# Optimization experiments

Hardware: AMD Instinct MI355X
Metric: run time of the kernel (lower is better)

Reference implementation:

```python
import jax, jax.numpy as jnp
import numpy as np

B, S, D, H, FF = 2, 2048, 1024, 16, 4096
HD = D // H
SCALE = 1.0 / np.sqrt(HD).astype(np.float32)
EPS = 1e-5


def _ln(x, g, b):
    m = jnp.mean(x, axis=-1, keepdims=True)
    v = jnp.mean((x - m) ** 2, axis=-1, keepdims=True)
    return (x - m) * jax.lax.rsqrt(v + EPS) * g + b


def setup_inputs() -> dict:
    key = jax.random.key(0)
    ks = jax.random.split(key, 8)
    def lin(k, fan_in, shape):
        return (jax.random.normal(k, shape, jnp.float32) / np.sqrt(fan_in)).astype(jnp.float32)
    return {
        "x": jax.random.normal(ks[0], (B, S, D), jnp.float32),
        "w_qkv": lin(ks[1], D, (D, 3 * D)),          # qkv_proj (no bias)
        "w_o": lin(ks[2], D, (D, D)),                 # out_proj
        "b_o": jnp.zeros((D,), jnp.float32),
        "g1": jnp.ones((D,), jnp.float32),            # attn LayerNorm
        "bt1": jnp.zeros((D,), jnp.float32),
        "w1": lin(ks[3], D, (D, FF)),                 # FFN linear1
        "b1": jnp.zeros((FF,), jnp.float32),
        "w2": lin(ks[4], FF, (FF, D)),                # FFN linear2
        "b2": jnp.zeros((D,), jnp.float32),
        "g2": jnp.ones((D,), jnp.float32),            # FFN LayerNorm
        "bt2": jnp.zeros((D,), jnp.float32),
    }


def reference(x, w_qkv, w_o, b_o, g1, bt1, w1, b1, w2, b2, g2, bt2):
    # --- MultiHeadAttention (post-LN, dropout=eval/identity) ---
    qkv = (x @ w_qkv).reshape(B, S, H, 3 * HD)
    q, k, v = jnp.split(qkv, 3, axis=-1)  # each [B,S,H,HD]
    # kernel_func = scaled softmax over keys
    scores = jnp.einsum("bihd,bjhd->bhij", q, k) * SCALE  # [B,H,S,S]
    attn = jax.nn.softmax(scores, axis=-1)
    ao = jnp.einsum("bhij,bjhd->bihd", attn, v).reshape(B, S, D)
    y = _ln(x + ao @ w_o + b_o, g1, bt1)
    # --- FFN (post-LN) ---
    h = jax.nn.relu(y @ w1 + b1)
    return _ln(y + h @ w2 + b2, g2, bt2)
```

## Files before the change

### kernel.cpp

```cpp
#include <hip/hip_runtime.h>
#include <hip/hip_bf16.h>

#define B_  2
#define S_  2048
#define D_  1024
#define H_  16
#define HD_ 64
#define FF_ 4096
#define NT  (B_ * S_)
#define SCALE_ 0.125f
#define KLOG2E 0.1803368801111f
#define EPS_  1e-5f

typedef __attribute__((ext_vector_type(8))) short bf16x8;
typedef __attribute__((ext_vector_type(4))) float f32x4;

__device__ inline short f2bf(float f) {
    __hip_bfloat16 h = __float2bfloat16(f);
    return __builtin_bit_cast(short, h);
}
__device__ inline float bf2f(unsigned short u) {
    __hip_bfloat16 h = __builtin_bit_cast(__hip_bfloat16, u);
    return __bfloat162float(h);
}
__device__ inline unsigned int pk2bf(float lo, float hi) {
    __hip_bfloat162 h = __float22bfloat162_rn(float2{lo, hi});
    const unsigned short l16 = __builtin_bit_cast(unsigned short, h.x);
    const unsigned short h16 = __builtin_bit_cast(unsigned short, h.y);
    return (unsigned int)l16 | ((unsigned int)h16 << 16);
}

#define GLOBAL_AS __attribute__((address_space(1)))
#define LDS_AS    __attribute__((address_space(3)))

struct DetectArgs { const unsigned short* p[12]; int n[12]; };

__global__ __launch_bounds__(256) void detect_kernel(DetectArgs a, int* flags) {
    const int t = blockIdx.x;
    const unsigned short* s = a.p[t];
    const int cnt = min(a.n[t], 16384);
    const int tid = threadIdx.x;
    int huge = 0, zeven = 0;
    for (int i = tid; i < cnt; i += 256) {
        const unsigned short v = s[i];
        const int e = (v >> 7) & 0xFF;
        if (e >= 142) huge++;
        if (((i & 1) == 0) && ((v & 0x7FFF) == 0)) zeven++;
    }
    __shared__ int sh, sz;
    if (tid == 0) { sh = 0; sz = 0; }
    __syncthreads();
    atomicAdd(&sh, huge);
    atomicAdd(&sz, zeven);
    __syncthreads();
    if (tid == 0) flags[t] = (sh > 0 || sz * 4 > cnt) ? 1 : 0;
}

struct VecArgs { const void* src[7]; float* dst[7]; int n[7]; int fidx[7]; };

__global__ __launch_bounds__(256) void conv_x_vecs_kernel(
    const void* __restrict__ src, unsigned short* __restrict__ dst, int n,
    VecArgs a, const int* __restrict__ flags)
{
    const int i = blockIdx.x * 256 + threadIdx.x;
    if (i < n) {
        if (flags[0])
            dst[i] = (unsigned short)f2bf(((const float*)src)[i]);
        else
            dst[i] = ((const unsigned short*)src)[i];
    }
    if (blockIdx.x < 7) {
        const int v = blockIdx.x;
        const int f = flags[a.fidx[v]];
        for (int j = threadIdx.x; j < a.n[v]; j += 256) {
            a.dst[v][j] = f ? ((const float*)a.src[v])[j]
                            : bf2f(((const unsigned short*)a.src[v])[j]);
        }
    }
}

struct TArgs {
    const void* src[4]; unsigned short* dst[4];
    int K[4], N[4], fidx[4], start[5];
};

__global__ __launch_bounds__(256) void conv_t_all_kernel(
    TArgs t, const int* __restrict__ flags)
{
    __shared__ short T[32][33];
    const int tile = blockIdx.x;
    int w = 0;
    if (tile >= t.start[1]) w = 1;
    if (tile >= t.start[2]) w = 2;
    if (tile >= t.start[3]) w = 3;
    const int rel = tile - t.start[w];
    const int K = t.K[w], N = t.N[w];
    const int tilesN = N / 32;
    const int kt = (rel / tilesN) * 32, nt = (rel % tilesN) * 32;
    const void* src = t.src[w];
    unsigned short* dst = t.dst[w];
    const int f = flags[t.fidx[w]];

    const int c  = threadIdx.x & 31;
    const int r0 = (threadIdx.x >> 5) * 4;
#pragma unroll
    for (int i = 0; i < 4; i++) {
        const int r = r0 + i;
        const size_t gi = (size_t)(kt + r) * N + nt + c;
        short v = f ? f2bf(((const float*)src)[gi])
                    : (short)((const unsigned short*)src)[gi];
        T[c][r] = v;
    }
    __syncthreads();
#pragma unroll
    for (int i = 0; i < 4; i++) {
        const int n = r0 + i;
        dst[(size_t)(nt + n) * K + kt + c] = (unsigned short)T[n][c];
    }
}

#define G256_STAGE(tile_)                                                     \
    do {                                                                      \
        char* sb_ = smem + (size_t)((tile_) & 3) * 32768;                     \
        const int kb_ = (tile_) << 5;                                         \
        __builtin_amdgcn_global_load_lds(                                     \
            (const GLOBAL_AS void*)(ag0 + kb_),                               \
            (LDS_AS void*)(sb_ + sdst2), 16, 0, 0);                           \
        __builtin_amdgcn_global_load_lds(                                     \
            (const GLOBAL_AS void*)(ag1 + kb_),                               \
            (LDS_AS void*)(sb_ + 8192 + sdst2), 16, 0, 0);                    \
        __builtin_amdgcn_global_load_lds(                                     \
            (const GLOBAL_AS void*)(bg0 + kb_),                               \
            (LDS_AS void*)(sb_ + 16384 + sdst2), 16, 0, 0);                   \
        __builtin_amdgcn_global_load_lds(                                     \
            (const GLOBAL_AS void*)(bg1 + kb_),                               \
            (LDS_AS void*)(sb_ + 24576 + sdst2), 16, 0, 0);                   \
    } while (0)

template<bool HAS_BIAS, bool RELU, bool QSCALE>
__global__ __launch_bounds__(512) void gemm256_kernel(
    const unsigned short* __restrict__ A,
    const unsigned short* __restrict__ Bt,
    const float* __restrict__ bias,
    unsigned short* __restrict__ out,
    int M, int N, int K)
{
    extern __shared__ char smem[];

    const int tid  = threadIdx.x;
    const int wave = tid >> 6;
    const int lane = tid & 63;
    const int quad = lane >> 4;
    const int l16  = lane & 15;
    const int wr   = wave >> 2;
    const int wc   = wave & 3;

    const int row0 = blockIdx.x * 256;
    const int col0 = blockIdx.y * 256;

    const int srow  = tid >> 2;
    const int sk    = (((tid & 3) ^ ((srow >> 1) & 3)) * 8);
    const int sdst2 = srow * 64 + (tid & 3) * 16;
    const unsigned short* ag0 = A  + (size_t)(row0 + srow) * K + sk;
    const unsigned short* ag1 = A  + (size_t)(row0 + 128 + srow) * K + sk;
    const unsigned short* bg0 = Bt + (size_t)(col0 + srow) * K + sk;
    const unsigned short* bg1 = Bt + (size_t)(col0 + 128 + srow) * K + sk;

    const int rsw = (quad ^ ((l16 >> 1) & 3)) * 8;

    const int NTk = K >> 5;

    f32x4 acc[8][4] = {};

    G256_STAGE(0);
    G256_STAGE(1);
    G256_STAGE(2);

    for (int t = 0; t < NTk; t++) {
        if (t + 2 < NTk)
            asm volatile("s_waitcnt vmcnt(8)\n\ts_barrier" ::: "memory");
        else if (t + 1 < NTk)
            asm volatile("s_waitcnt vmcnt(4)\n\ts_barrier" ::: "memory");
        else
            asm volatile("s_waitcnt vmcnt(0)\n\ts_barrier" ::: "memory");

        const short* sA = (const short*)(smem + (size_t)(t & 3) * 32768);
        const short* sB = sA + 8192;

        bf16x8 af[8], bfr[4];
#pragma unroll
        for (int mi = 0; mi < 8; mi++)
            af[mi] = *reinterpret_cast<const bf16x8*>(
                &sA[(wr * 128 + mi * 16 + l16) * 32 + rsw]);
#pragma unroll
        for (int ni = 0; ni < 4; ni++)
            bfr[ni] = *reinterpret_cast<const bf16x8*>(
                &sB[(wc * 64 + ni * 16 + l16) * 32 + rsw]);
#pragma unroll
        for (int mi = 0; mi < 8; mi++)
#pragma unroll
            for (int ni = 0; ni < 4; ni++)
                acc[mi][ni] = __builtin_amdgcn_mfma_f32_16x16x32_bf16(
                    af[mi], bfr[ni], acc[mi][ni], 0, 0, 0);

        if (t + 3 < NTk) G256_STAGE(t + 3);
    }

#pragma unroll
    for (int ni = 0; ni < 4; ni++) {
        const int col = col0 + wc * 64 + ni * 16 + l16;
        float badd = 0.f;
        if constexpr (HAS_BIAS) badd = bias[col];
        float qs = 1.f;
        if constexpr (QSCALE)
            qs = (((col0 + wc * 64 + ni * 16) % 192) < 64) ? KLOG2E : 1.f;
#pragma unroll
        for (int mi = 0; mi < 8; mi++) {
#pragma unroll
            for (int r = 0; r < 4; r++) {
                const int row = row0 + wr * 128 + mi * 16 + quad * 4 + r;
                float v = acc[mi][ni][r] + badd;
                if constexpr (QSCALE) v *= qs;
                if constexpr (RELU) v = fmaxf(v, 0.f);
                out[(size_t)row * N + col] = (unsigned short)f2bf(v);
            }
        }
    }
}

#define GSK_STAGE(tile_)                                                      \
    do {                                                                      \
        char* sb_ = smem + (size_t)((tile_) & 3) * 16384;                     \
        const int kb_ = (tile_) << 5;                                         \
        __builtin_amdgcn_global_load_lds(                                     \
            (const GLOBAL_AS void*)(agp0 + kb_),                              \
            (LDS_AS void*)(sb_ + adst0), 16, 0, 0);                           \
        __builtin_amdgcn_global_load_lds(                                     \
            (const GLOBAL_AS void*)(agp1 + kb_),                              \
            (LDS_AS void*)(sb_ + adst1), 16, 0, 0);                           \
        __builtin_amdgcn_global_load_lds(                                     \
            (const GLOBAL_AS void*)(bgp0 + kb_),                              \
            (LDS_AS void*)(sb_ + 8192 + adst0), 16, 0, 0);                    \
        __builtin_amdgcn_global_load_lds(                                     \
            (const GLOBAL_AS void*)(bgp1 + kb_),                              \
            (LDS_AS void*)(sb_ + 8192 + adst1), 16, 0, 0);                    \
    } while (0)

__global__ __launch_bounds__(256) void gemm128_sk_kernel(
    const unsigned short* __restrict__ A,
    const unsigned short* __restrict__ Bt,
    float* __restrict__ out0,
    float* __restrict__ out1,
    int M, int N, int K)
{
    extern __shared__ char smem[];

    const int tid  = threadIdx.x;
    const int wave = tid >> 6;
    const int lane = tid & 63;
    const int quad = lane >> 4;
    const int l16  = lane & 15;

    const int row0 = blockIdx.x * 128;
    const int col0 = blockIdx.y * 128;
    const int z    = blockIdx.z;
    const int Kh   = K >> 1;

    const unsigned short* Az  = A  + (size_t)z * Kh;
    const unsigned short* Btz = Bt + (size_t)z * Kh;
    float* out = z ? out1 : out0;

    const int ldrow = lane >> 2;
    const int ldk   = (((lane & 3) ^ ((ldrow >> 1) & 3)) * 8);
    const unsigned short* agp0 = Az  + (size_t)(row0 + wave * 32 + ldrow) * K + ldk;
    const unsigned short* agp1 = agp0 + (size_t)16 * K;
    const unsigned short* bgp0 = Btz + (size_t)(col0 + wave * 32 + ldrow) * K + ldk;
    const unsigned short* bgp1 = bgp0 + (size_t)16 * K;

    const int adst0 = (wave * 32 + ldrow) * 64 + (lane & 3) * 16;
    const int adst1 = adst0 + 16 * 64;

    const int wm = (wave >> 1) * 64;
    const int wn = (wave & 1) * 64;
    const int rsw = (quad ^ ((l16 >> 1) & 3)) * 8;

    const int NTk = Kh >> 5;

    f32x4 acc[4][4] = {};

    GSK_STAGE(0);
    if (1 < NTk) GSK_STAGE(1);
    if (2 < NTk) GSK_STAGE(2);

    for (int t = 0; t < NTk; t++) {
        if (t + 2 < NTk)
            asm volatile("s_waitcnt vmcnt(8)\n\ts_barrier" ::: "memory");
        else if (t + 1 < NTk)
            asm volatile("s_waitcnt vmcnt(4)\n\ts_barrier" ::: "memory");
        else
            asm volatile("s_waitcnt vmcnt(0)\n\ts_barrier" ::: "memory");

        const short* sA = (const short*)(smem + (size_t)(t & 3) * 16384);
        const short* sB = sA + 4096;

        bf16x8 af[4], bfr[4];
#pragma unroll
        for (int mi = 0; mi < 4; mi++)
            af[mi] = *reinterpret_cast<const bf16x8*>(
                &sA[(wm + mi * 16 + l16) * 32 + rsw]);
#pragma unroll
        for (int ni = 0; ni < 4; ni++)
            bfr[ni] = *reinterpret_cast<const bf16x8*>(
                &sB[(wn + ni * 16 + l16) * 32 + rsw]);
#pragma unroll
        for (int mi = 0; mi < 4; mi++)
#pragma unroll
            for (int ni = 0; ni < 4; ni++)
                acc[mi][ni] = __builtin_amdgcn_mfma_f32_16x16x32_bf16(
                    af[mi], bfr[ni], acc[mi][ni], 0, 0, 0);

        if (t + 3 < NTk) GSK_STAGE(t + 3);
    }

#pragma unroll
    for (int ni = 0; ni < 4; ni++) {
        const int col = col0 + wn + ni * 16 + l16;
#pragma unroll
        for (int mi = 0; mi < 4; mi++)
#pragma unroll
            for (int r = 0; r < 4; r++) {
                const int row = row0 + wm + mi * 16 + quad * 4 + r;
                out[(size_t)row * N + col] = acc[mi][ni][r];
            }
    }
}

__global__ __launch_bounds__(512) void attn_kernel(
    const unsigned short* __restrict__ qkv,
    unsigned short* __restrict__ ao)
{
    extern __shared__ char smem[];

    const int qt = blockIdx.x;
    const int h  = blockIdx.y;
    const int b  = blockIdx.z;

    const int tid  = threadIdx.x;
    const int wave = tid >> 6;
    const int g    = wave >> 2;
    const int gw   = wave & 3;
    const int lane = tid & 63;
    const int quad = lane >> 4;
    const int l16  = lane & 15;
    const int gtid = tid & 255;

    short* Ks = (short*)smem + g * (64 * 72);
    short* Vt = (short*)(smem + 18432) + g * (64 * 72);
    short* Ps = (short*)(smem + 36864) + wave * (32 * 72);

    bf16x8 qf[2][2];
#pragma unroll
    for (int mi = 0; mi < 2; mi++) {
        const int qrow = qt * 128 + gw * 32 + mi * 16 + l16;
        const unsigned short* qb = qkv + (size_t)(b * S_ + qrow) * 3072 + h * 192;
        qf[mi][0] = *reinterpret_cast<const bf16x8*>(qb + quad * 8);
        qf[mi][1] = *reinterpret_cast<const bf16x8*>(qb + 32 + quad * 8);
    }

    bf16x8 vones;
#pragma unroll
    for (int j = 0; j < 8; j++) vones[j] = (short)0x3F80;

    f32x4 o[2][4] = {};
    f32x4 o_l[2] = {};

    const int skey = gtid >> 3;
    const int soct = gtid & 7;
    const int vp   = gtid >> 3;
    const int kA   = (vp & 15) + ((vp >> 4) << 5);
    const int kB   = kA + 16;
    const int posA = 4 * (vp & 15) + 2 * (vp >> 4);
    const int vwr  = ((posA >> 3) ^ soct) * 8 + (posA & 7);

    const int kb0   = g * (S_ / 2);
    const int kbend = kb0 + S_ / 2;

    const unsigned short* kbase0 = qkv + (size_t)(b * S_) * 3072 + h * 192 + 64;
    const unsigned short* vbase0 = qkv + (size_t)(b * S_) * 3072 + h * 192 + 128;

    bf16x8 pk0 = *reinterpret_cast<const bf16x8*>(kbase0 + (size_t)(kb0 + skey) * 3072 + soct * 8);
    bf16x8 pk1 = *reinterpret_cast<const bf16x8*>(kbase0 + (size_t)(kb0 + skey + 32) * 3072 + soct * 8);
    bf16x8 pv0 = *reinterpret_cast<const bf16x8*>(vbase0 + (size_t)(kb0 + kA) * 3072 + soct * 8);
    bf16x8 pv1 = *reinterpret_cast<const bf16x8*>(vbase0 + (size_t)(kb0 + kB) * 3072 + soct * 8);

    for (int kb = kb0; kb < kbend; kb += 64) {
        {
            const int woct0 = soct ^ ((skey >> 3) & 1);
            *reinterpret_cast<bf16x8*>(&Ks[skey * 72 + woct0 * 8]) = pk0;
            const int woct1 = soct ^ (((skey + 32) >> 3) & 1);
            *reinterpret_cast<bf16x8*>(&Ks[(skey + 32) * 72 + woct1 * 8]) = pk1;
#pragma unroll
            for (int j = 0; j < 8; j++) {
                const int d = soct * 8 + j;
                const unsigned int val =
                    (unsigned int)(unsigned short)pv0[j] |
                    ((unsigned int)(unsigned short)pv1[j] << 16);
                *reinterpret_cast<unsigned int*>(&Vt[d * 72 + vwr]) = val;
            }
        }
        __syncthreads();

        {
            const int kbn = (kb + 64 < kbend) ? kb + 64 : kb;
            pk0 = *reinterpret_cast<const bf16x8*>(
                kbase0 + (size_t)(kbn + skey) * 3072 + soct * 8);
            pk1 = *reinterpret_cast<const bf16x8*>(
                kbase0 + (size_t)(kbn + skey + 32) * 3072 + soct * 8);
            pv0 = *reinterpret_cast<const bf16x8*>(
                vbase0 + (size_t)(kbn + kA) * 3072 + soct * 8);
            pv1 = *reinterpret_cast<const bf16x8*>(
                vbase0 + (size_t)(kbn + kB) * 3072 + soct * 8);
        }

        f32x4 s[2][4] = {};
#pragma unroll
        for (int c2 = 0; c2 < 2; c2++) {
#pragma unroll
            for (int nt = 0; nt < 4; nt++) {
                const int key = nt * 16 + l16;
                const int roct = (c2 * 4 + quad) ^ ((key >> 3) & 1);
                bf16x8 kf = *reinterpret_cast<const bf16x8*>(
                    &Ks[key * 72 + roct * 8]);
                s[0][nt] = __builtin_amdgcn_mfma_f32_16x16x32_bf16(qf[0][c2], kf, s[0][nt], 0, 0, 0);
                s[1][nt] = __builtin_amdgcn_mfma_f32_16x16x32_bf16(qf[1][c2], kf, s[1][nt], 0, 0, 0);
            }
        }

#pragma unroll
        for (int mi = 0; mi < 2; mi++) {
#pragma unroll
            for (int r = 0; r < 4; r++) {
                const int m = mi * 16 + quad * 4 + r;
                const float p0 = exp2f(s[mi][0][r]);
                const float p1 = exp2f(s[mi][1][r]);
                const float p2 = exp2f(s[mi][2][r]);
                const float p3 = exp2f(s[mi][3][r]);
                uint2 w;
                w.x = pk2bf(p0, p1);
                w.y = pk2bf(p2, p3);
                *reinterpret_cast<uint2*>(&Ps[m * 72 + l16 * 4]) = w;
            }
        }

#pragma unroll
        for (int c2 = 0; c2 < 2; c2++) {
            bf16x8 pf[2];
#pragma unroll
            for (int mi = 0; mi < 2; mi++) {
                const int m = mi * 16 + l16;
                pf[mi] = *reinterpret_cast<const bf16x8*>(
                    &Ps[m * 72 + c2 * 32 + quad * 8]);
            }
#pragma unroll
            for (int ct = 0; ct < 4; ct++) {
                const int row = ct * 16 + l16;
                const int blk = (c2 * 4 + quad) ^ (row >> 3);
                bf16x8 vf = *reinterpret_cast<const bf16x8*>(
                    &Vt[row * 72 + blk * 8]);
                o[0][ct] = __builtin_amdgcn_mfma_f32_16x16x32_bf16(pf[0], vf, o[0][ct], 0, 0, 0);
                o[1][ct] = __builtin_amdgcn_mfma_f32_16x16x32_bf16(pf[1], vf, o[1][ct], 0, 0, 0);
            }
            o_l[0] = __builtin_amdgcn_mfma_f32_16x16x32_bf16(pf[0], vones, o_l[0], 0, 0, 0);
            o_l[1] = __builtin_amdgcn_mfma_f32_16x16x32_bf16(pf[1], vones, o_l[1], 0, 0, 0);
        }
        __syncthreads();
    }

    float* ex = (float*)smem;
    const int slot = (gw * 64 + lane) * 40;
    if (g == 1) {
#pragma unroll
        for (int mi = 0; mi < 2; mi++) {
#pragma unroll
            for (int ct = 0; ct < 4; ct++)
                *reinterpret_cast<f32x4*>(&ex[slot + mi * 16 + ct * 4]) = o[mi][ct];
            *reinterpret_cast<f32x4*>(&ex[slot + 32 + mi * 4]) = o_l[mi];
        }
    }
    __syncthreads();
    if (g == 0) {
#pragma unroll
        for (int mi = 0; mi < 2; mi++) {
#pragma unroll
            for (int ct = 0; ct < 4; ct++) {
                f32x4 t = *reinterpret_cast<const f32x4*>(&ex[slot + mi * 16 + ct * 4]);
                o[mi][ct] += t;
            }
            f32x4 tl = *reinterpret_cast<const f32x4*>(&ex[slot + 32 + mi * 4]);
            o_l[mi] += tl;
        }
#pragma unroll
        for (int mi = 0; mi < 2; mi++) {
            f32x4 rl;
#pragma unroll
            for (int r = 0; r < 4; r++) rl[r] = 1.f / o_l[mi][r];
#pragma unroll
            for (int ct = 0; ct < 4; ct++)
#pragma unroll
                for (int r = 0; r < 4; r++) {
                    const int row = qt * 128 + gw * 32 + mi * 16 + quad * 4 + r;
                    ao[(size_t)(b * S_ + row) * D_ + h * HD_ + ct * 16 + l16] =
                        (unsigned short)f2bf(o[mi][ct][r] * rl[r]);
                }
        }
    }
}

template<int RESM, bool FLAG_OUT>
__global__ __launch_bounds__(256) void ln_sum_kernel(
    const float* __restrict__ p0,
    const float* __restrict__ p1,
    const float* __restrict__ bias,
    const unsigned short* __restrict__ resb,
    const float* __restrict__ resf,
    const float* __restrict__ g,
    const float* __restrict__ bt,
    const int* __restrict__ flags,
    void* __restrict__ out)
{
    const int row = blockIdx.x;
    const int tid = threadIdx.x;
    const int c0  = tid * 4;
    const size_t base = (size_t)row * D_ + c0;

    float4 a = *reinterpret_cast<const float4*>(p0 + base);
    float4 bq = *reinterpret_cast<const float4*>(p1 + base);
    float4 bi = *reinterpret_cast<const float4*>(bias + c0);

    float v[4] = {a.x + bq.x + bi.x, a.y + bq.y + bi.y,
                  a.z + bq.z + bi.z, a.w + bq.w + bi.w};

    if constexpr (RESM == 1) {
        if (flags[0]) {
            float4 rv = *reinterpret_cast<const float4*>(resf + base);
            v[0] += rv.x; v[1] += rv.y; v[2] += rv.z; v[3] += rv.w;
        } else {
            uint2 rv = *reinterpret_cast<const uint2*>(resb + base);
            v[0] += bf2f((unsigned short)(rv.x & 0xFFFF));
            v[1] += bf2f((unsigned short)(rv.x >> 16));
            v[2] += bf2f((unsigned short)(rv.y & 0xFFFF));
            v[3] += bf2f((unsigned short)(rv.y >> 16));
        }
    } else {
        uint2 rv = *reinterpret_cast<const uint2*>(resb + base);
        v[0] += bf2f((unsigned short)(rv.x & 0xFFFF));
        v[1] += bf2f((unsigned short)(rv.x >> 16));
        v[2] += bf2f((unsigned short)(rv.y & 0xFFFF));
        v[3] += bf2f((unsigned short)(rv.y >> 16));
    }

    float s = v[0] + v[1] + v[2] + v[3];
    float sq = v[0] * v[0] + v[1] * v[1] + v[2] * v[2] + v[3] * v[3];
#pragma unroll
    for (int msk = 1; msk < 64; msk <<= 1) {
        s += __shfl_xor(s, msk);
        sq += __shfl_xor(sq, msk);
    }
    __shared__ float ss[4], ssq[4];
    if ((tid & 63) == 0) { ss[tid >> 6] = s; ssq[tid >> 6] = sq; }
    __syncthreads();
    s = ss[0] + ss[1] + ss[2] + ss[3];
    sq = ssq[0] + ssq[1] + ssq[2] + ssq[3];

    const float mean = s * (1.f / D_);
    const float var = sq * (1.f / D_) - mean * mean;
    const float rinv = rsqrtf(var + EPS_);

    float w[4];
#pragma unroll
    for (int i = 0; i < 4; i++)
        w[i] = (v[i] - mean) * rinv * g[c0 + i] + bt[c0 + i];

    int outF32 = 0;
    if constexpr (FLAG_OUT) outF32 = flags[0];

    if (FLAG_OUT && outF32) {
        float4 o4 = {w[0], w[1], w[2], w[3]};
        *reinterpret_cast<float4*>((float*)out + base) = o4;
    } else {
        uint2 o2;
        o2.x = pk2bf(w[0], w[1]);
        o2.y = pk2bf(w[2], w[3]);
        *reinterpret_cast<uint2*>((unsigned short*)out + base) = o2;
    }
}

extern "C" void kernel_launch(void* const* d_in, const int* in_sizes, int n_in,
                              void* d_out, int out_size, void* d_ws, size_t ws_size,
                              hipStream_t stream) {
    char* ws = (char*)d_ws;

    int*            flags = (int*)(ws + 0);
    unsigned short* xb    = (unsigned short*)(ws + 256);
    unsigned short* wqkvT = (unsigned short*)(ws + 8388864);
    unsigned short* woT   = (unsigned short*)(ws + 14680320);
    unsigned short* w1T   = (unsigned short*)(ws + 16777472);
    unsigned short* w2T   = (unsigned short*)(ws + 25166080);
    float*          bof   = (float*)(ws + 33554688);
    float*          g1f   = (float*)(ws + 33558784);
    float*          bt1f  = (float*)(ws + 33562880);
    float*          b1f   = (float*)(ws + 33566976);
    float*          b2f   = (float*)(ws + 33583360);
    float*          g2f   = (float*)(ws + 33587456);
    float*          bt2f  = (float*)(ws + 33591552);
    unsigned short* qkv   = (unsigned short*)(ws + 33595648);
    unsigned short* ao    = (unsigned short*)(ws + 256);
    unsigned short* y     = (unsigned short*)(ws + 33595648);
    unsigned short* hbuf  = (unsigned short*)(ws + 41984256);
    float*          part0 = (float*)(ws + 58761472);
    float*          part1 = (float*)(ws + 75538688);
    float*          hpart0= (float*)(ws + 256);

    dim3 blk(256);

    static int attr_done = 0;
    if (!attr_done) {
        hipFuncSetAttribute(reinterpret_cast<const void*>(attn_kernel),
                            hipFuncAttributeMaxDynamicSharedMemorySize, 73728);
        hipFuncSetAttribute(
            reinterpret_cast<const void*>(&gemm256_kernel<false, false, true>),
            hipFuncAttributeMaxDynamicSharedMemorySize, 131072);
        hipFuncSetAttribute(
            reinterpret_cast<const void*>(&gemm256_kernel<true, true, false>),
            hipFuncAttributeMaxDynamicSharedMemorySize, 131072);
        hipFuncSetAttribute(reinterpret_cast<const void*>(gemm128_sk_kernel),
                            hipFuncAttributeMaxDynamicSharedMemorySize, 65536);
        attr_done = 1;
    }

    DetectArgs da;
    for (int i = 0; i < 12; i++) {
        da.p[i] = (const unsigned short*)d_in[i];
        da.n[i] = in_sizes[i];
    }
    detect_kernel<<<dim3(12), blk, 0, stream>>>(da, flags);

    VecArgs va;
    const int vidx[7] = {3, 4, 5, 7, 9, 10, 11};
    float* vdst[7] = {bof, g1f, bt1f, b1f, b2f, g2f, bt2f};
    for (int i = 0; i < 7; i++) {
        va.src[i] = d_in[vidx[i]];
        va.dst[i] = vdst[i];
        va.n[i]   = in_sizes[vidx[i]];
        va.fidx[i] = vidx[i];
    }
    conv_x_vecs_kernel<<<dim3((NT * D_ + 255) / 256), blk, 0, stream>>>(
        d_in[0], xb, NT * D_, va, flags);

    TArgs ta;
    ta.src[0] = d_in[1]; ta.dst[0] = wqkvT; ta.K[0] = D_;  ta.N[0] = 3 * D_; ta.fidx[0] = 1;
    ta.src[1] = d_in[2]; ta.dst[1] = woT;   ta.K[1] = D_;  ta.N[1] = D_;     ta.fidx[1] = 2;
    ta.src[2] = d_in[6]; ta.dst[2] = w1T;   ta.K[2] = D_;  ta.N[2] = FF_;    ta.fidx[2] = 6;
    ta.src[3] = d_in[8]; ta.dst[3] = w2T;   ta.K[3] = FF_; ta.N[3] = D_;     ta.fidx[3] = 8;
    ta.start[0] = 0;
    for (int wI = 0; wI < 4; wI++)
        ta.start[wI + 1] = ta.start[wI] + (ta.K[wI] / 32) * (ta.N[wI] / 32);
    conv_t_all_kernel<<<dim3(ta.start[4]), blk, 0, stream>>>(ta, flags);

    gemm256_kernel<false, false, true>
        <<<dim3(NT / 256, 3072 / 256), dim3(512), 131072, stream>>>(
            xb, wqkvT, nullptr, qkv, NT, 3072, 1024);

    attn_kernel<<<dim3(S_ / 128, H_, B_), dim3(512), 73728, stream>>>(qkv, ao);

    gemm128_sk_kernel<<<dim3(NT / 128, 1024 / 128, 2), blk, 65536, stream>>>(
        ao, woT, part0, part1, NT, 1024, 1024);

    ln_sum_kernel<1, false><<<dim3(NT), blk, 0, stream>>>(
        part0, part1, bof, (const unsigned short*)d_in[0], (const float*)d_in[0],
        g1f, bt1f, flags, y);

    gemm256_kernel<true, true, false>
        <<<dim3(NT / 256, 4096 / 256), dim3(512), 131072, stream>>>(
            y, w1T, b1f, hbuf, NT, 4096, 1024);

    gemm128_sk_kernel<<<dim3(NT / 128, 1024 / 128, 2), blk, 65536, stream>>>(
        hbuf, w2T, hpart0, part1, NT, 1024, 4096);

    ln_sum_kernel<2, true><<<dim3(NT), blk, 0, stream>>>(
        hpart0, part1, b2f, y, nullptr, g2f, bt2f, flags, d_out);
}
```

Baseline: 372.5 us.

## Keep attention probabilities in registers by transposing the QK MFMA

Swaps the MFMA operand order for the score computation so each lane ends up holding the P values in the layout the PV MFMA needs as its A operand. The probabilities are packed to bf16 in registers, which removes the per-wave LDS staging buffer for P and its write/read round trip. The V transpose write permutation is changed to match the new key ordering, and dynamic shared memory drops from 73728 to 40960 bytes, which may allow more blocks per CU. The risk is a mismatch between the key permutation in V and the register layout of P, which would give wrong results.

```diff
diff --git a/kernel.cpp b/kernel.cpp
--- a/kernel.cpp
+++ b/kernel.cpp
@@ -14,6 +14,7 @@
 
 typedef __attribute__((ext_vector_type(8))) short bf16x8;
 typedef __attribute__((ext_vector_type(4))) float f32x4;
+typedef __attribute__((ext_vector_type(4))) unsigned int u32x4;
 
 __device__ inline short f2bf(float f) {
     __hip_bfloat16 h = __float2bfloat16(f);
@@ -356,7 +357,6 @@
 
     short* Ks = (short*)smem + g * (64 * 72);
     short* Vt = (short*)(smem + 18432) + g * (64 * 72);
-    short* Ps = (short*)(smem + 36864) + wave * (32 * 72);
 
     bf16x8 qf[2][2];
 #pragma unroll
@@ -377,9 +377,11 @@
     const int skey = gtid >> 3;
     const int soct = gtid & 7;
     const int vp   = gtid >> 3;
-    const int kA   = (vp & 15) + ((vp >> 4) << 5);
-    const int kB   = kA + 16;
-    const int posA = 4 * (vp & 15) + 2 * (vp >> 4);
+    const int kA   = ((vp >> 1) << 2) + ((vp & 1) << 1);
+    const int kB   = kA + 1;
+    const int ntA  = kA >> 4;
+    const int posA = ((ntA >> 1) << 5) + (((kA >> 2) & 3) << 3)
+                   + ((ntA & 1) << 2) + (kA & 3);
     const int vwr  = ((posA >> 3) ^ soct) * 8 + (posA & 7);
 
     const int kb0   = g * (S_ / 2);
@@ -431,35 +433,30 @@
                 const int roct = (c2 * 4 + quad) ^ ((key >> 3) & 1);
                 bf16x8 kf = *reinterpret_cast<const bf16x8*>(
                     &Ks[key * 72 + roct * 8]);
-                s[0][nt] = __builtin_amdgcn_mfma_f32_16x16x32_bf16(qf[0][c2], kf, s[0][nt], 0, 0, 0);
-                s[1][nt] = __builtin_amdgcn_mfma_f32_16x16x32_bf16(qf[1][c2], kf, s[1][nt], 0, 0, 0);
+                s[0][nt] = __builtin_amdgcn_mfma_f32_16x16x32_bf16(kf, qf[0][c2], s[0][nt], 0, 0, 0);
+                s[1][nt] = __builtin_amdgcn_mfma_f32_16x16x32_bf16(kf, qf[1][c2], s[1][nt], 0, 0, 0);
             }
         }
 
 #pragma unroll
-        for (int mi = 0; mi < 2; mi++) {
-#pragma unroll
-            for (int r = 0; r < 4; r++) {
-                const int m = mi * 16 + quad * 4 + r;
-                const float p0 = exp2f(s[mi][0][r]);
-                const float p1 = exp2f(s[mi][1][r]);
-                const float p2 = exp2f(s[mi][2][r]);
-                const float p3 = exp2f(s[mi][3][r]);
-                uint2 w;
-                w.x = pk2bf(p0, p1);
-                w.y = pk2bf(p2, p3);
-                *reinterpret_cast<uint2*>(&Ps[m * 72 + l16 * 4]) = w;
-            }
-        }
+        for (int mi = 0; mi < 2; mi++)
+#pragma unroll
+            for (int nt = 0; nt < 4; nt++)
+#pragma unroll
+                for (int r = 0; r < 4; r++)
+                    s[mi][nt][r] = exp2f(s[mi][nt][r]);
 
 #pragma unroll
         for (int c2 = 0; c2 < 2; c2++) {
             bf16x8 pf[2];
 #pragma unroll
             for (int mi = 0; mi < 2; mi++) {
-                const int m = mi * 16 + l16;
-                pf[mi] = *reinterpret_cast<const bf16x8*>(
-                    &Ps[m * 72 + c2 * 32 + quad * 8]);
+                u32x4 w;
+                w[0] = pk2bf(s[mi][2 * c2][0],     s[mi][2 * c2][1]);
+                w[1] = pk2bf(s[mi][2 * c2][2],     s[mi][2 * c2][3]);
+                w[2] = pk2bf(s[mi][2 * c2 + 1][0], s[mi][2 * c2 + 1][1]);
+                w[3] = pk2bf(s[mi][2 * c2 + 1][2], s[mi][2 * c2 + 1][3]);
+                pf[mi] = __builtin_bit_cast(bf16x8, w);
             }
 #pragma unroll
             for (int ct = 0; ct < 4; ct++) {
@@ -625,8 +622,6 @@
 
     static int attr_done = 0;
     if (!attr_done) {
-        hipFuncSetAttribute(reinterpret_cast<const void*>(attn_kernel),
-                            hipFuncAttributeMaxDynamicSharedMemorySize, 73728);
         hipFuncSetAttribute(
             reinterpret_cast<const void*>(&gemm256_kernel<false, false, true>),
             hipFuncAttributeMaxDynamicSharedMemorySize, 131072);
@@ -671,7 +666,7 @@
         <<<dim3(NT / 256, 3072 / 256), dim3(512), 131072, stream>>>(
             xb, wqkvT, nullptr, qkv, NT, 3072, 1024);
 
-    attn_kernel<<<dim3(S_ / 128, H_, B_), dim3(512), 73728, stream>>>(qkv, ao);
+    attn_kernel<<<dim3(S_ / 128, H_, B_), dim3(512), 40960, stream>>>(qkv, ao);
 
     gemm128_sk_kernel<<<dim3(NT / 128, 1024 / 128, 2), blk, 65536, stream>>>(
         ao, woT, part0, part1, NT, 1024, 1024);
```

Measured after the change: 387.1 us. +3.9%, slower.
